# Performance work log

Hardware: AMD Instinct MI355X
Metric: run time of the kernel (lower is better)

## Reference

```python
import jax, jax.numpy as jnp
import numpy as np

N_P, N_D = 100000, 50000
C, S, H = 128, 128, 128
E = 600000


def setup_inputs() -> dict:
    key = jax.random.key(0)
    ks = jax.random.split(key, 20)
    sc = 1.0 / np.sqrt(H)
    inp = {
        "h_p": jax.random.normal(ks[0], (N_P, C), dtype=jnp.float32),
        "h_d": jax.random.normal(ks[1], (N_D, S), dtype=jnp.float32),
        "pd_src": jax.random.randint(ks[2], (E,), 0, N_P),
        "pd_dst": jax.random.randint(ks[3], (E,), 0, N_D),
        "dp_src": jax.random.randint(ks[4], (E,), 0, N_D),
        "dp_dst": jax.random.randint(ks[5], (E,), 0, N_P),
    }
    names = [("W1_pd", (C, H)), ("W1_dp", (S, H)), ("W2_pd", (H, H)),
             ("W2_dp", (H, H)), ("W3_pd", (H, S)), ("W3_dp", (H, C))]
    for i, (nm, shp) in enumerate(names):
        inp[nm] = jax.random.normal(ks[6 + i], shp, dtype=jnp.float32) * sc
        inp["b" + nm[1:]] = jnp.zeros((shp[1],), dtype=jnp.float32)
    return inp


def gconv(x, src, dst, n_dst, W, b):
    """DGL GraphConv, norm='both': relu(D_dst^-1/2 A D_src^-1/2 X W + b)."""
    n_src = x.shape[0]
    ones = jnp.ones(src.shape, dtype=x.dtype)
    deg_out = jnp.maximum(jax.ops.segment_sum(ones, src, num_segments=n_src), 1.0)
    deg_in = jnp.maximum(jax.ops.segment_sum(ones, dst, num_segments=n_dst), 1.0)
    xs = x * jax.lax.rsqrt(deg_out)[:, None]
    m = jax.ops.segment_sum(xs[src], dst, num_segments=n_dst)  # [n_dst, d_in]
    m = m * jax.lax.rsqrt(deg_in)[:, None]
    return jax.nn.relu(m @ W + b)


def reference(h_p, h_d, pd_src, pd_dst, dp_src, dp_dst,
              W1_pd, b1_pd, W1_dp, b1_dp,
              W2_pd, b2_pd, W2_dp, b2_dp,
              W3_pd, b3_pd, W3_dp, b3_dp):
    # Layer 1: p_d sends p feats to d; d_p sends d feats to p
    h_d1 = gconv(h_p, pd_src, pd_dst, N_D, W1_pd, b1_pd)
    h_p1 = gconv(h_d, dp_src, dp_dst, N_P, W1_dp, b1_dp)
    # Layer 2
    h_d2 = gconv(h_p1, pd_src, pd_dst, N_D, W2_pd, b2_pd)
    h_p2 = gconv(h_d1, dp_src, dp_dst, N_P, W2_dp, b2_dp)
    # Layer 3: d gets S-dim, p gets C-dim
    h_d3 = gconv(h_p2, pd_src, pd_dst, N_D, W3_pd, b3_pd)
    h_p3 = gconv(h_d2, dp_src, dp_dst, N_P, W3_dp, b3_dp)
    return h_p3, h_d3
```

## Files before the change

kernel.cpp:

```cpp
#include <hip/hip_runtime.h>
#include <stdint.h>

#define N_P 100000
#define N_D 50000
#define NE  600000
#define F   128
#define FP  136

#define NCHK   32
#define CHKE   18752
#define HPARTS 16
#define HPART_P (N_P/HPARTS)
#define HPART_D (N_D/HPARTS)
#define HOFS_A0 ((size_t)0)
#define HOFS_A1 ((size_t)32*N_P)
#define HOFS_A2 ((size_t)32*N_P + (size_t)32*N_D)
#define HOFS_A3 ((size_t)32*N_P + (size_t)64*N_D)

typedef __attribute__((ext_vector_type(8))) __bf16 bf16x8;
typedef __attribute__((ext_vector_type(4))) float  f32x4;

static __device__ __forceinline__ float bf2f(uint16_t u){
  union{float f;uint32_t i;} v; v.i = ((uint32_t)u)<<16; return v.f;
}
static __device__ __forceinline__ uint16_t f2bf(float f){
  union{float f;uint32_t i;} v; v.f = f;
  uint32_t i = v.i;
  uint32_t r = i + 0x7fffu + ((i>>16)&1u);
  return (uint16_t)(r>>16);
}

__global__ __launch_bounds__(256) void k_hist(
    const int* __restrict__ pd_src, const int* __restrict__ pd_dst,
    const int* __restrict__ dp_src, const int* __restrict__ dp_dst,
    int* __restrict__ hist){
  __shared__ int cnt[HPART_P];
  const int b = blockIdx.x;
  const int arr = b >> 9, part = (b >> 5) & 15, chunk = b & 31;
  const int* src; int N; size_t hofs;
  switch(arr){
    case 0:  src = pd_src; N = N_P; hofs = HOFS_A0; break;
    case 1:  src = pd_dst; N = N_D; hofs = HOFS_A1; break;
    case 2:  src = dp_src; N = N_D; hofs = HOFS_A2; break;
    default: src = dp_dst; N = N_P; hofs = HOFS_A3; break;
  }
  const int PART = N / HPARTS;
  const int lo = part * PART;
  for (int i = threadIdx.x; i < PART; i += 256) cnt[i] = 0;
  __syncthreads();
  const int e0 = chunk*CHKE, e1 = min(e0 + CHKE, NE);
  const uint4* s4 = (const uint4*)(src + e0);
  const int n4 = (e1 - e0) >> 2;
  for (int i = threadIdx.x; i < n4; i += 256){
    uint4 v = s4[i];
    int a0 = (int)v.x - lo, a1 = (int)v.y - lo, a2 = (int)v.z - lo, a3 = (int)v.w - lo;
    if ((unsigned)a0 < (unsigned)PART) atomicAdd(&cnt[a0], 1);
    if ((unsigned)a1 < (unsigned)PART) atomicAdd(&cnt[a1], 1);
    if ((unsigned)a2 < (unsigned)PART) atomicAdd(&cnt[a2], 1);
    if ((unsigned)a3 < (unsigned)PART) atomicAdd(&cnt[a3], 1);
  }
  __syncthreads();
  int* out = hist + hofs + (size_t)chunk*N + lo;
  for (int i = threadIdx.x; i < PART; i += 256) out[i] = cnt[i];
}

__global__ void k_sumdeg(int* __restrict__ hist,
                         int* __restrict__ cnt_d_in, int* __restrict__ cnt_p_in,
                         float* __restrict__ rs_p_out, float* __restrict__ rs_p_in,
                         float* __restrict__ rs_d_out, float* __restrict__ rs_d_in){
  const int idx = blockIdx.x*256 + threadIdx.x;
  const int arr = blockIdx.y;
  int N; size_t hofs; bool pre;
  switch(arr){
    case 0:  N = N_P; hofs = HOFS_A0; pre = false; break;
    case 1:  N = N_D; hofs = HOFS_A1; pre = true;  break;
    case 2:  N = N_D; hofs = HOFS_A2; pre = false; break;
    default: N = N_P; hofs = HOFS_A3; pre = true;  break;
  }
  if (idx >= N) return;
  int* base = hist + hofs + idx;
  int run = 0;
  if (pre){
    #pragma unroll 4
    for (int c = 0; c < NCHK; ++c){
      int v = base[(size_t)c*N]; base[(size_t)c*N] = run; run += v;
    }
  } else {
    #pragma unroll 4
    for (int c = 0; c < NCHK; ++c) run += base[(size_t)c*N];
  }
  float rs = rsqrtf((float)max(run, 1));
  switch(arr){
    case 0:  rs_p_out[idx] = rs; break;
    case 1:  cnt_d_in[idx] = run; rs_d_in[idx] = rs; break;
    case 2:  rs_d_out[idx] = rs; break;
    default: cnt_p_in[idx] = run; rs_p_in[idx] = rs; break;
  }
}

__global__ void k_scan1(const int* __restrict__ cA, int nA,
                        const int* __restrict__ cB, int nB,
                        int* __restrict__ bsums, int nbA){
  __shared__ int red[8];
  int b = blockIdx.x, t = threadIdx.x;
  const int* in; int n, bi, slot;
  if (b < nbA){ in = cA; n = nA; bi = b;       slot = bi; }
  else        { in = cB; n = nB; bi = b - nbA; slot = 256 + bi; }
  int i = bi*512 + t;
  int v = (i < n) ? in[i] : 0;
  #pragma unroll
  for (int o = 32; o; o >>= 1) v += __shfl_down(v, o, 64);
  if ((t & 63) == 0) red[t >> 6] = v;
  __syncthreads();
  if (t == 0){ int s = 0; for (int k = 0; k < 8; ++k) s += red[k]; bsums[slot] = s; }
}

__global__ void k_scan2(int* bsums, int nbA, int nbB){
  __shared__ int sh[256];
  int seg = blockIdx.x, t = threadIdx.x;
  int nb = seg ? nbB : nbA;
  int* p = bsums + seg*256;
  int v = (t < nb) ? p[t] : 0;
  sh[t] = v; __syncthreads();
  for (int ofs = 1; ofs < 256; ofs <<= 1){
    int u = (t >= ofs) ? sh[t-ofs] : 0; __syncthreads();
    sh[t] += u; __syncthreads();
  }
  if (t < nb) p[t] = sh[t] - v;
}

__global__ void k_scan3(const int* __restrict__ cA, int nA,
                        const int* __restrict__ cB, int nB,
                        const int* __restrict__ bsums, int nbA,
                        int* __restrict__ offA, int* __restrict__ offB){
  __shared__ int sh[512];
  int b = blockIdx.x, t = threadIdx.x;
  const int* in; int n, bi; int* out; int base;
  if (b < nbA){ in = cA; n = nA; bi = b;       out = offA; base = bsums[bi]; }
  else        { in = cB; n = nB; bi = b - nbA; out = offB; base = bsums[256+bi]; }
  int i = bi*512 + t;
  int v = (i < n) ? in[i] : 0;
  sh[t] = v; __syncthreads();
  for (int ofs = 1; ofs < 512; ofs <<= 1){
    int u = (t >= ofs) ? sh[t-ofs] : 0; __syncthreads();
    sh[t] += u; __syncthreads();
  }
  if (i < n) out[i] = base + sh[t] - v;
  if (b == 0 && t == 0){ offA[nA] = NE; offB[nB] = NE; }
}

__global__ __launch_bounds__(256) void k_scatter(
    const int* __restrict__ pd_src, const int* __restrict__ pd_dst,
    const int* __restrict__ dp_src, const int* __restrict__ dp_dst,
    const int* __restrict__ off_pd, const int* __restrict__ off_dp,
    const int* __restrict__ hist,
    int* __restrict__ col_pd, int* __restrict__ col_dp){
  __shared__ int base[HPART_P];
  __shared__ int fill[HPART_P];
  const int b = blockIdx.x;
  const int gph = b >> 9, part = (b >> 5) & 15, chunk = b & 31;
  const int* dsts; const int* srcs; const int* off; int* col; int N; size_t hofs;
  if (gph == 0){ dsts = pd_dst; srcs = pd_src; off = off_pd; col = col_pd; N = N_D; hofs = HOFS_A1; }
  else         { dsts = dp_dst; srcs = dp_src; off = off_dp; col = col_dp; N = N_P; hofs = HOFS_A3; }
  const int PART = N / HPARTS;
  const int lo = part * PART;
  const int* hc   = hist + hofs + (size_t)chunk*N + lo;
  const int* offp = off + lo;
  for (int i = threadIdx.x; i < PART; i += 256){ base[i] = offp[i] + hc[i]; fill[i] = 0; }
  __syncthreads();
  const int e0 = chunk*CHKE, e1 = min(e0 + CHKE, NE);
  const uint4* d4 = (const uint4*)(dsts + e0);
  const int n4 = (e1 - e0) >> 2;
  for (int i = threadIdx.x; i < n4; i += 256){
    uint4 d = d4[i];
    int a0 = (int)d.x - lo, a1 = (int)d.y - lo, a2 = (int)d.z - lo, a3 = (int)d.w - lo;
    int e = e0 + 4*i;
    if ((unsigned)a0 < (unsigned)PART){ int r = atomicAdd(&fill[a0], 1); col[base[a0] + r] = srcs[e+0]; }
    if ((unsigned)a1 < (unsigned)PART){ int r = atomicAdd(&fill[a1], 1); col[base[a1] + r] = srcs[e+1]; }
    if ((unsigned)a2 < (unsigned)PART){ int r = atomicAdd(&fill[a2], 1); col[base[a2] + r] = srcs[e+2]; }
    if ((unsigned)a3 < (unsigned)PART){ int r = atomicAdd(&fill[a3], 1); col[base[a3] + r] = srcs[e+3]; }
  }
}

__global__ void k_convert(const float4* __restrict__ hp, const float4* __restrict__ hd,
                          const float* __restrict__ rs_po, const float* __restrict__ rs_do,
                          uint2* __restrict__ P0, uint2* __restrict__ D0){
  int i = blockIdx.x*256 + threadIdx.x;
  const int nP4 = N_P*F/4, nD4 = N_D*F/4;
  if (i < nP4){
    float4 v = hp[i]; float s = rs_po[i >> 5];
    uint2 r;
    r.x = ((uint32_t)f2bf(v.y*s)<<16) | f2bf(v.x*s);
    r.y = ((uint32_t)f2bf(v.w*s)<<16) | f2bf(v.z*s);
    P0[i] = r;
  } else {
    int j = i - nP4;
    if (j < nD4){
      float4 v = hd[j]; float s = rs_do[j >> 5];
      uint2 r;
      r.x = ((uint32_t)f2bf(v.y*s)<<16) | f2bf(v.x*s);
      r.y = ((uint32_t)f2bf(v.w*s)<<16) | f2bf(v.z*s);
      D0[j] = r;
    }
  }
}

__global__ void k_prepw(const float* w0,const float* w1,const float* w2,
                        const float* w3,const float* w4,const float* w5,
                        uint16_t* __restrict__ wt,
                        uint16_t* z0, uint16_t* z1, uint16_t* z2,
                        uint16_t* z3, uint16_t* z4, uint16_t* z5){
  int m = blockIdx.x;
  const float* W; uint16_t* Z;
  switch(m){ case 0:W=w0;Z=z0;break; case 1:W=w1;Z=z1;break; case 2:W=w2;Z=z2;break;
             case 3:W=w3;Z=z3;break; case 4:W=w4;Z=z4;break; default:W=w5;Z=z5; }
  uint16_t* T = wt + m*F*FP;
  for (int idx = threadIdx.x; idx < F*F; idx += 256){
    int k = idx >> 7, j = idx & 127;
    T[j*FP + k] = f2bf(W[idx]);
  }
  if (threadIdx.x < F) Z[threadIdx.x] = 0;
}

template<int OUT_MODE>
__global__ __launch_bounds__(256, 7) void k_gconv2(
    const uint16_t* __restrict__ xA, const int* __restrict__ offAp, const int* __restrict__ colA,
    const float* __restrict__ rsA, const uint16_t* __restrict__ WtA, const float* __restrict__ biasA,
    const float* __restrict__ rsnA, void* __restrict__ outA, int ndA, int nsA, int nblkA,
    const uint16_t* __restrict__ xB, const int* __restrict__ offBp, const int* __restrict__ colB,
    const float* __restrict__ rsB, const uint16_t* __restrict__ WtB, const float* __restrict__ biasB,
    const float* __restrict__ rsnB, void* __restrict__ outB, int ndB, int nsB)
{
  __shared__ uint16_t m_lds[64*FP];
  const int tid  = threadIdx.x;
  const int lane = tid & 63;
  const int wv   = tid >> 6;

  const uint16_t* x; const int* off; const int* col; const float* rs_in;
  const uint16_t* Wt; const float* bias; const float* rs_next; void* outp;
  int n_dst, zrow, bid;
  if ((int)blockIdx.x < nblkA){
    x = xA; off = offAp; col = colA; rs_in = rsA; Wt = WtA; bias = biasA;
    rs_next = rsnA; outp = outA; n_dst = ndA; zrow = nsA; bid = blockIdx.x;
  } else {
    x = xB; off = offBp; col = colB; rs_in = rsB; Wt = WtB; bias = biasB;
    rs_next = rsnB; outp = outB; n_dst = ndB; zrow = nsB; bid = blockIdx.x - nblkA;
  }

  const int row0 = bid*64 + wv*16;
  const int g    = lane >> 4;
  const int l    = lane & 15;
  #pragma unroll
  for (int i = 0; i < 4; ++i){
    int r = row0 + i*4 + g;
    bool rv = r < n_dst;
    int e0 = rv ? off[r]   : 0;
    int e1 = rv ? off[r+1] : 0;
    float a0=0.f,a1=0.f,a2=0.f,a3=0.f,a4=0.f,a5=0.f,a6=0.f,a7=0.f;
    for (int e = e0; e < e1; e += 16){
      int idx = e + l;
      int cv  = col[idx < e1 ? idx : e1-1];
      int cnt = e1 - e;
      #pragma unroll
      for (int h = 0; h < 2; ++h){
        if (h*8 < cnt){
          #pragma unroll
          for (int q = h*8; q < h*8 + 8; ++q){
            int c = __shfl(cv, g*16 + q, 64);
            c = (q < cnt) ? c : zrow;
            uint4 u = *(const uint4*)(x + (size_t)c*F + l*8);
            a0 += bf2f((uint16_t)u.x); a1 += bf2f((uint16_t)(u.x>>16));
            a2 += bf2f((uint16_t)u.y); a3 += bf2f((uint16_t)(u.y>>16));
            a4 += bf2f((uint16_t)u.z); a5 += bf2f((uint16_t)(u.z>>16));
            a6 += bf2f((uint16_t)u.w); a7 += bf2f((uint16_t)(u.w>>16));
          }
        }
      }
    }
    float rs = rv ? rs_in[r] : 0.f;
    uint4 pk;
    pk.x = ((uint32_t)f2bf(a1*rs)<<16) | f2bf(a0*rs);
    pk.y = ((uint32_t)f2bf(a3*rs)<<16) | f2bf(a2*rs);
    pk.z = ((uint32_t)f2bf(a5*rs)<<16) | f2bf(a4*rs);
    pk.w = ((uint32_t)f2bf(a7*rs)<<16) | f2bf(a6*rs);
    *(uint4*)&m_lds[(wv*16 + i*4 + g)*FP + l*8] = pk;
  }
  __syncthreads();

  f32x4 acc[8];
  #pragma unroll
  for (int t = 0; t < 8; ++t) acc[t] = (f32x4){0.f,0.f,0.f,0.f};
  const int mrow = lane & 15;
  const int kgrp = lane >> 4;
  #pragma unroll
  for (int k0 = 0; k0 < F; k0 += 32){
    bf16x8 a = *(const bf16x8*)&m_lds[(wv*16 + mrow)*FP + k0 + kgrp*8];
    #pragma unroll
    for (int t = 0; t < 8; ++t){
      bf16x8 b = *(const bf16x8*)&Wt[(t*16 + mrow)*FP + k0 + kgrp*8];
      acc[t] = __builtin_amdgcn_mfma_f32_16x16x32_bf16(a, b, acc[t], 0, 0, 0);
    }
  }

  float bv[8];
  #pragma unroll
  for (int t = 0; t < 8; ++t) bv[t] = bias[t*16 + mrow];
  #pragma unroll
  for (int reg = 0; reg < 4; ++reg){
    int rr = row0 + kgrp*4 + reg;
    if (rr < n_dst){
      float rsn = (OUT_MODE == 0) ? rs_next[rr] : 0.f;
      #pragma unroll
      for (int t = 0; t < 8; ++t){
        int n = t*16 + mrow;
        float v = acc[t][reg] + bv[t];
        v = fmaxf(v, 0.f);
        if (OUT_MODE == 0){
          ((uint16_t*)outp)[rr*F + n] = f2bf(v * rsn);
        } else {
          ((float*)outp)[rr*F + n] = v;
        }
      }
    }
  }
}

extern "C" void kernel_launch(void* const* d_in, const int* in_sizes, int n_in,
                              void* d_out, int out_size, void* d_ws, size_t ws_size,
                              hipStream_t stream) {
  const float* h_p   = (const float*)d_in[0];
  const float* h_d   = (const float*)d_in[1];
  const int* pd_src  = (const int*)d_in[2];
  const int* pd_dst  = (const int*)d_in[3];
  const int* dp_src  = (const int*)d_in[4];
  const int* dp_dst  = (const int*)d_in[5];
  const float* W1_pd = (const float*)d_in[6];   const float* b1_pd = (const float*)d_in[7];
  const float* W1_dp = (const float*)d_in[8];   const float* b1_dp = (const float*)d_in[9];
  const float* W2_pd = (const float*)d_in[10];  const float* b2_pd = (const float*)d_in[11];
  const float* W2_dp = (const float*)d_in[12];  const float* b2_dp = (const float*)d_in[13];
  const float* W3_pd = (const float*)d_in[14];  const float* b3_pd = (const float*)d_in[15];
  const float* W3_dp = (const float*)d_in[16];  const float* b3_dp = (const float*)d_in[17];

  char* w = (char*)d_ws;
  size_t o = 0;
  auto take = [&](size_t bytes)->char*{
    char* p = w + o; o += (bytes + 255) & ~(size_t)255; return p;
  };

  int* cnt_d_in  = (int*)take(4*(size_t)N_D);
  int* cnt_p_in  = (int*)take(4*(size_t)N_P);
  int* off_pd   = (int*)take(4*(size_t)(N_D+1));
  int* off_dp   = (int*)take(4*(size_t)(N_P+1));
  int* bsums    = (int*)take(4*512);
  int* col_pd   = (int*)take(4*(size_t)NE);
  int* col_dp   = (int*)take(4*(size_t)NE);
  float* rs_p_out = (float*)take(4*(size_t)N_P);
  float* rs_p_in  = (float*)take(4*(size_t)N_P);
  float* rs_d_out = (float*)take(4*(size_t)N_D);
  float* rs_d_in  = (float*)take(4*(size_t)N_D);
  uint16_t* wt  = (uint16_t*)take(2*(size_t)6*F*FP);
  uint16_t* P0  = (uint16_t*)take(2*(size_t)(N_P+1)*F);
  uint16_t* P1  = (uint16_t*)take(2*(size_t)(N_P+1)*F);
  uint16_t* P2  = (uint16_t*)take(2*(size_t)(N_P+1)*F);
  uint16_t* D0  = (uint16_t*)take(2*(size_t)(N_D+1)*F);
  uint16_t* D1  = (uint16_t*)take(2*(size_t)(N_D+1)*F);
  uint16_t* D2  = (uint16_t*)take(2*(size_t)(N_D+1)*F);

  int* hist = (int*)P1;

  k_hist<<<4*HPARTS*NCHK, 256, 0, stream>>>(pd_src, pd_dst, dp_src, dp_dst, hist);
  k_sumdeg<<<dim3((N_P+255)/256, 4), 256, 0, stream>>>(
      hist, cnt_d_in, cnt_p_in, rs_p_out, rs_p_in, rs_d_out, rs_d_in);
  const int nbA = (N_D + 511)/512;
  const int nbB = (N_P + 511)/512;
  k_scan1<<<nbA+nbB, 512, 0, stream>>>(cnt_d_in, N_D, cnt_p_in, N_P, bsums, nbA);
  k_scan2<<<2, 256, 0, stream>>>(bsums, nbA, nbB);
  k_scan3<<<nbA+nbB, 512, 0, stream>>>(cnt_d_in, N_D, cnt_p_in, N_P, bsums, nbA, off_pd, off_dp);
  k_scatter<<<2*HPARTS*NCHK, 256, 0, stream>>>(pd_src, pd_dst, dp_src, dp_dst,
                                               off_pd, off_dp, hist, col_pd, col_dp);
  k_convert<<<((N_P+N_D)*F/4 + 255)/256, 256, 0, stream>>>(
      (const float4*)h_p, (const float4*)h_d, rs_p_out, rs_d_out, (uint2*)P0, (uint2*)D0);
  k_prepw<<<6, 256, 0, stream>>>(W1_pd, W1_dp, W2_pd, W2_dp, W3_pd, W3_dp, wt,
                                 P0 + (size_t)N_P*F, D0 + (size_t)N_D*F,
                                 P1 + (size_t)N_P*F, D1 + (size_t)N_D*F,
                                 P2 + (size_t)N_P*F, D2 + (size_t)N_D*F);

  const int gd = (N_D + 63)/64, gp = (N_P + 63)/64;
  k_gconv2<0><<<gd+gp, 256, 0, stream>>>(
      P0, off_pd, col_pd, rs_d_in, wt + 0*F*FP, b1_pd, rs_d_out, D1, N_D, N_P, gd,
      D0, off_dp, col_dp, rs_p_in, wt + 1*F*FP, b1_dp, rs_p_out, P1, N_P, N_D);
  k_gconv2<0><<<gd+gp, 256, 0, stream>>>(
      P1, off_pd, col_pd, rs_d_in, wt + 2*F*FP, b2_pd, rs_d_out, D2, N_D, N_P, gd,
      D1, off_dp, col_dp, rs_p_in, wt + 3*F*FP, b2_dp, rs_p_out, P2, N_P, N_D);
  k_gconv2<1><<<gd+gp, 256, 0, stream>>>(
      P2, off_pd, col_pd, rs_d_in, wt + 4*F*FP, b3_pd, nullptr, (float*)d_out + (size_t)N_P*F, N_D, N_P, gd,
      D2, off_dp, col_dp, rs_p_in, wt + 5*F*FP, b3_dp, nullptr, (float*)d_out, N_P, N_D);
}
```

Baseline: 533.5 us.

## Prefetch neighbor indices, swap MFMA operands for vector stores, merge weight prep

Several changes at once. The gather loop now prefetches the next batch of column indices ahead of the feature loads, and the initial column loads for all four rows are issued up front. MFMA operands are swapped so each lane holds four consecutive output columns, which allows packed uint2/float4 stores and vectorised bias loads; the __syncthreads is dropped because each wave only reads its own LDS rows. The histogram and scatter kernels use half as many partitions, and scatter increments base directly instead of keeping a separate fill array. The weight-prep kernel is folded into the convert kernel to save one launch. Halving the partitions doubles per-block LDS and work, which risks lower occupancy in those kernels.

```diff
diff --git a/kernel.cpp b/kernel.cpp
--- a/kernel.cpp
+++ b/kernel.cpp
@@ -9,7 +9,7 @@
 
 #define NCHK   32
 #define CHKE   18752
-#define HPARTS 16
+#define HPARTS 8
 #define HPART_P (N_P/HPARTS)
 #define HPART_D (N_D/HPARTS)
 #define HOFS_A0 ((size_t)0)
@@ -36,7 +36,7 @@
     int* __restrict__ hist){
   __shared__ int cnt[HPART_P];
   const int b = blockIdx.x;
-  const int arr = b >> 9, part = (b >> 5) & 15, chunk = b & 31;
+  const int arr = b >> 8, part = (b >> 5) & 7, chunk = b & 31;
   const int* src; int N; size_t hofs;
   switch(arr){
     case 0:  src = pd_src; N = N_P; hofs = HOFS_A0; break;
@@ -156,9 +156,8 @@
     const int* __restrict__ hist,
     int* __restrict__ col_pd, int* __restrict__ col_dp){
   __shared__ int base[HPART_P];
-  __shared__ int fill[HPART_P];
   const int b = blockIdx.x;
-  const int gph = b >> 9, part = (b >> 5) & 15, chunk = b & 31;
+  const int gph = b >> 8, part = (b >> 5) & 7, chunk = b & 31;
   const int* dsts; const int* srcs; const int* off; int* col; int N; size_t hofs;
   if (gph == 0){ dsts = pd_dst; srcs = pd_src; off = off_pd; col = col_pd; N = N_D; hofs = HOFS_A1; }
   else         { dsts = dp_dst; srcs = dp_src; off = off_dp; col = col_dp; N = N_P; hofs = HOFS_A3; }
@@ -166,7 +165,7 @@
   const int lo = part * PART;
   const int* hc   = hist + hofs + (size_t)chunk*N + lo;
   const int* offp = off + lo;
-  for (int i = threadIdx.x; i < PART; i += 256){ base[i] = offp[i] + hc[i]; fill[i] = 0; }
+  for (int i = threadIdx.x; i < PART; i += 256) base[i] = offp[i] + hc[i];
   __syncthreads();
   const int e0 = chunk*CHKE, e1 = min(e0 + CHKE, NE);
   const uint4* d4 = (const uint4*)(dsts + e0);
@@ -175,17 +174,35 @@
     uint4 d = d4[i];
     int a0 = (int)d.x - lo, a1 = (int)d.y - lo, a2 = (int)d.z - lo, a3 = (int)d.w - lo;
     int e = e0 + 4*i;
-    if ((unsigned)a0 < (unsigned)PART){ int r = atomicAdd(&fill[a0], 1); col[base[a0] + r] = srcs[e+0]; }
-    if ((unsigned)a1 < (unsigned)PART){ int r = atomicAdd(&fill[a1], 1); col[base[a1] + r] = srcs[e+1]; }
-    if ((unsigned)a2 < (unsigned)PART){ int r = atomicAdd(&fill[a2], 1); col[base[a2] + r] = srcs[e+2]; }
-    if ((unsigned)a3 < (unsigned)PART){ int r = atomicAdd(&fill[a3], 1); col[base[a3] + r] = srcs[e+3]; }
+    if ((unsigned)a0 < (unsigned)PART){ int p = atomicAdd(&base[a0], 1); col[p] = srcs[e+0]; }
+    if ((unsigned)a1 < (unsigned)PART){ int p = atomicAdd(&base[a1], 1); col[p] = srcs[e+1]; }
+    if ((unsigned)a2 < (unsigned)PART){ int p = atomicAdd(&base[a2], 1); col[p] = srcs[e+2]; }
+    if ((unsigned)a3 < (unsigned)PART){ int p = atomicAdd(&base[a3], 1); col[p] = srcs[e+3]; }
   }
 }
 
 __global__ void k_convert(const float4* __restrict__ hp, const float4* __restrict__ hd,
                           const float* __restrict__ rs_po, const float* __restrict__ rs_do,
-                          uint2* __restrict__ P0, uint2* __restrict__ D0){
-  int i = blockIdx.x*256 + threadIdx.x;
+                          uint2* __restrict__ P0, uint2* __restrict__ D0,
+                          const float* w0,const float* w1,const float* w2,
+                          const float* w3,const float* w4,const float* w5,
+                          uint16_t* __restrict__ wt,
+                          uint16_t* z0, uint16_t* z1, uint16_t* z2,
+                          uint16_t* z3, uint16_t* z4, uint16_t* z5){
+  if (blockIdx.x < 6){
+    int m = blockIdx.x;
+    const float* W; uint16_t* Z;
+    switch(m){ case 0:W=w0;Z=z0;break; case 1:W=w1;Z=z1;break; case 2:W=w2;Z=z2;break;
+               case 3:W=w3;Z=z3;break; case 4:W=w4;Z=z4;break; default:W=w5;Z=z5; }
+    uint16_t* T = wt + m*F*FP;
+    for (int idx = threadIdx.x; idx < F*F; idx += 256){
+      int k = idx >> 7, j = idx & 127;
+      T[j*FP + k] = f2bf(W[idx]);
+    }
+    if (threadIdx.x < F) Z[threadIdx.x] = 0;
+    return;
+  }
+  int i = (blockIdx.x - 6)*256 + threadIdx.x;
   const int nP4 = N_P*F/4, nD4 = N_D*F/4;
   if (i < nP4){
     float4 v = hp[i]; float s = rs_po[i >> 5];
@@ -205,23 +222,6 @@
   }
 }
 
-__global__ void k_prepw(const float* w0,const float* w1,const float* w2,
-                        const float* w3,const float* w4,const float* w5,
-                        uint16_t* __restrict__ wt,
-                        uint16_t* z0, uint16_t* z1, uint16_t* z2,
-                        uint16_t* z3, uint16_t* z4, uint16_t* z5){
-  int m = blockIdx.x;
-  const float* W; uint16_t* Z;
-  switch(m){ case 0:W=w0;Z=z0;break; case 1:W=w1;Z=z1;break; case 2:W=w2;Z=z2;break;
-             case 3:W=w3;Z=z3;break; case 4:W=w4;Z=z4;break; default:W=w5;Z=z5; }
-  uint16_t* T = wt + m*F*FP;
-  for (int idx = threadIdx.x; idx < F*F; idx += 256){
-    int k = idx >> 7, j = idx & 127;
-    T[j*FP + k] = f2bf(W[idx]);
-  }
-  if (threadIdx.x < F) Z[threadIdx.x] = 0;
-}
-
 template<int OUT_MODE>
 __global__ __launch_bounds__(256, 7) void k_gconv2(
     const uint16_t* __restrict__ xA, const int* __restrict__ offAp, const int* __restrict__ colA,
@@ -250,17 +250,31 @@
   const int row0 = bid*64 + wv*16;
   const int g    = lane >> 4;
   const int l    = lane & 15;
+
+  int e0a[4], e1a[4], cva[4];
   #pragma unroll
   for (int i = 0; i < 4; ++i){
     int r = row0 + i*4 + g;
     bool rv = r < n_dst;
-    int e0 = rv ? off[r]   : 0;
-    int e1 = rv ? off[r+1] : 0;
+    e0a[i] = rv ? off[r]   : 0;
+    e1a[i] = rv ? off[r+1] : 0;
+  }
+  #pragma unroll
+  for (int i = 0; i < 4; ++i){
+    int last = (e1a[i] > 0) ? e1a[i]-1 : 0;
+    int idx  = e0a[i] + l;
+    cva[i] = col[idx < e1a[i] ? idx : last];
+  }
+
+  #pragma unroll
+  for (int i = 0; i < 4; ++i){
+    int e0 = e0a[i], e1 = e1a[i];
+    int cv = cva[i];
     float a0=0.f,a1=0.f,a2=0.f,a3=0.f,a4=0.f,a5=0.f,a6=0.f,a7=0.f;
     for (int e = e0; e < e1; e += 16){
-      int idx = e + l;
-      int cv  = col[idx < e1 ? idx : e1-1];
-      int cnt = e1 - e;
+      int nidx = e + 16 + l;
+      int ncv  = col[nidx < e1 ? nidx : e1-1];
+      int cnt  = e1 - e;
       #pragma unroll
       for (int h = 0; h < 2; ++h){
         if (h*8 < cnt){
@@ -276,8 +290,10 @@
           }
         }
       }
-    }
-    float rs = rv ? rs_in[r] : 0.f;
+      cv = ncv;
+    }
+    int r = row0 + i*4 + g;
+    float rs = (r < n_dst) ? rs_in[r] : 0.f;
     uint4 pk;
     pk.x = ((uint32_t)f2bf(a1*rs)<<16) | f2bf(a0*rs);
     pk.y = ((uint32_t)f2bf(a3*rs)<<16) | f2bf(a2*rs);
@@ -285,7 +301,6 @@
     pk.w = ((uint32_t)f2bf(a7*rs)<<16) | f2bf(a6*rs);
     *(uint4*)&m_lds[(wv*16 + i*4 + g)*FP + l*8] = pk;
   }
-  __syncthreads();
 
   f32x4 acc[8];
   #pragma unroll
@@ -294,32 +309,33 @@
   const int kgrp = lane >> 4;
   #pragma unroll
   for (int k0 = 0; k0 < F; k0 += 32){
-    bf16x8 a = *(const bf16x8*)&m_lds[(wv*16 + mrow)*FP + k0 + kgrp*8];
+    bf16x8 bfrag = *(const bf16x8*)&m_lds[(wv*16 + mrow)*FP + k0 + kgrp*8];
     #pragma unroll
     for (int t = 0; t < 8; ++t){
-      bf16x8 b = *(const bf16x8*)&Wt[(t*16 + mrow)*FP + k0 + kgrp*8];
-      acc[t] = __builtin_amdgcn_mfma_f32_16x16x32_bf16(a, b, acc[t], 0, 0, 0);
-    }
-  }
-
-  float bv[8];
-  #pragma unroll
-  for (int t = 0; t < 8; ++t) bv[t] = bias[t*16 + mrow];
-  #pragma unroll
-  for (int reg = 0; reg < 4; ++reg){
-    int rr = row0 + kgrp*4 + reg;
-    if (rr < n_dst){
-      float rsn = (OUT_MODE == 0) ? rs_next[rr] : 0.f;
-      #pragma unroll
-      for (int t = 0; t < 8; ++t){
-        int n = t*16 + mrow;
-        float v = acc[t][reg] + bv[t];
-        v = fmaxf(v, 0.f);
-        if (OUT_MODE == 0){
-          ((uint16_t*)outp)[rr*F + n] = f2bf(v * rsn);
-        } else {
-          ((float*)outp)[rr*F + n] = v;
-        }
+      bf16x8 afrag = *(const bf16x8*)&Wt[(t*16 + mrow)*FP + k0 + kgrp*8];
+      acc[t] = __builtin_amdgcn_mfma_f32_16x16x32_bf16(afrag, bfrag, acc[t], 0, 0, 0);
+    }
+  }
+
+  const int q4 = kgrp * 4;
+  const int rr = row0 + mrow;
+  if (rr < n_dst){
+    float rsn = (OUT_MODE == 0) ? rs_next[rr] : 1.f;
+    #pragma unroll
+    for (int t = 0; t < 8; ++t){
+      float4 b4 = *(const float4*)&bias[t*16 + q4];
+      float v0 = fmaxf(acc[t][0] + b4.x, 0.f);
+      float v1 = fmaxf(acc[t][1] + b4.y, 0.f);
+      float v2 = fmaxf(acc[t][2] + b4.z, 0.f);
+      float v3 = fmaxf(acc[t][3] + b4.w, 0.f);
+      if (OUT_MODE == 0){
+        uint2 pk;
+        pk.x = ((uint32_t)f2bf(v1*rsn)<<16) | f2bf(v0*rsn);
+        pk.y = ((uint32_t)f2bf(v3*rsn)<<16) | f2bf(v2*rsn);
+        *(uint2*)((uint16_t*)outp + (size_t)rr*F + t*16 + q4) = pk;
+      } else {
+        float4 o; o.x = v0; o.y = v1; o.z = v2; o.w = v3;
+        *(float4*)((float*)outp + (size_t)rr*F + t*16 + q4) = o;
       }
     }
   }
@@ -378,12 +394,12 @@
   k_scan3<<<nbA+nbB, 512, 0, stream>>>(cnt_d_in, N_D, cnt_p_in, N_P, bsums, nbA, off_pd, off_dp);
   k_scatter<<<2*HPARTS*NCHK, 256, 0, stream>>>(pd_src, pd_dst, dp_src, dp_dst,
                                                off_pd, off_dp, hist, col_pd, col_dp);
-  k_convert<<<((N_P+N_D)*F/4 + 255)/256, 256, 0, stream>>>(
-      (const float4*)h_p, (const float4*)h_d, rs_p_out, rs_d_out, (uint2*)P0, (uint2*)D0);
-  k_prepw<<<6, 256, 0, stream>>>(W1_pd, W1_dp, W2_pd, W2_dp, W3_pd, W3_dp, wt,
-                                 P0 + (size_t)N_P*F, D0 + (size_t)N_D*F,
-                                 P1 + (size_t)N_P*F, D1 + (size_t)N_D*F,
-                                 P2 + (size_t)N_P*F, D2 + (size_t)N_D*F);
+  k_convert<<<((N_P+N_D)*F/4 + 255)/256 + 6, 256, 0, stream>>>(
+      (const float4*)h_p, (const float4*)h_d, rs_p_out, rs_d_out, (uint2*)P0, (uint2*)D0,
+      W1_pd, W1_dp, W2_pd, W2_dp, W3_pd, W3_dp, wt,
+      P0 + (size_t)N_P*F, D0 + (size_t)N_D*F,
+      P1 + (size_t)N_P*F, D1 + (size_t)N_D*F,
+      P2 + (size_t)N_P*F, D2 + (size_t)N_D*F);
 
   const int gd = (N_D + 63)/64, gp = (N_P + 63)/64;
   k_gconv2<0><<<gd+gp, 256, 0, stream>>>(
```

Measured after the change: 517.1 us. -3.1%, faster.
